# Performance work log

Measured on AMD Instinct MI355X. Metric: run time of the kernel, lower is better.

## Reference

```python
import jax, jax.numpy as jnp
import numpy as np

NUM_NODES = 25
EMBED_DIM = 64
OUT_SIZE = 2
N_TOTAL = 204800   # 8192 graphs * 25 nodes
N_EDGES = 3276800  # avg degree 16


def setup_inputs() -> dict:
    key = jax.random.key(0)
    ks = jax.random.split(key, 8)
    x = jax.random.normal(ks[0], (N_TOTAL, EMBED_DIM), dtype=jnp.float32)
    # random edges; real graphs are graph-local but math is identical
    edge_index = jax.random.randint(ks[1], (2, N_EDGES), 0, N_TOTAL, dtype=jnp.int32)
    batch = jnp.repeat(jnp.arange(N_TOTAL // NUM_NODES, dtype=jnp.int32), NUM_NODES)
    hid = NUM_NODES * EMBED_DIM  # 1600
    W_conv = jax.random.normal(ks[2], (EMBED_DIM, EMBED_DIM), dtype=jnp.float32) / np.sqrt(EMBED_DIM)
    b_conv = jnp.zeros((EMBED_DIM,), dtype=jnp.float32)
    W1 = jax.random.normal(ks[3], (hid, hid), dtype=jnp.float32) / np.sqrt(hid)
    b1 = jnp.zeros((hid,), dtype=jnp.float32)
    W2 = jax.random.normal(ks[4], (hid, OUT_SIZE), dtype=jnp.float32) / np.sqrt(hid)
    b2 = jnp.zeros((OUT_SIZE,), dtype=jnp.float32)
    return {"x": x, "edge_index": edge_index, "batch": batch,
            "W_conv": W_conv, "b_conv": b_conv,
            "W1": W1, "b1": b1, "W2": W2, "b2": b2}


def reference(x, edge_index, batch, W_conv, b_conv, W1, b1, W2, b2):
    N = x.shape[0]
    # --- GCNConv: add self-loops, symmetric degree norm, transform, scatter-add ---
    loop = jnp.arange(N, dtype=edge_index.dtype)
    src = jnp.concatenate([edge_index[0], loop])
    dst = jnp.concatenate([edge_index[1], loop])
    deg = jax.ops.segment_sum(jnp.ones_like(dst, dtype=x.dtype), dst, num_segments=N)
    dinv = jax.lax.rsqrt(deg)  # deg >= 1 due to self-loops
    norm = dinv[src] * dinv[dst]                       # [E+N]
    h = x @ W_conv                                     # [N, D]
    msg = h[src] * norm[:, None]                       # gather + scale
    h = jax.ops.segment_sum(msg, dst, num_segments=N) + b_conv
    h = jax.nn.relu(h)
    # --- dense head ---
    nb = -(-batch.shape[0] // NUM_NODES)               # ceil
    h = h.reshape(nb, NUM_NODES * EMBED_DIM)           # [B, 1600]
    h = jax.nn.relu(h @ W1 + b1)
    logits = h @ W2 + b2
    return jax.nn.softmax(logits, axis=-1)
```

## Files before the change

### kernel.cpp

```cpp
#include <hip/hip_runtime.h>
#include <hip/hip_bf16.h>
#include <stdint.h>

#define NT   204800
#define NE   3276800
#define ED   64
#define NBG  8192
#define HID  1600
#define CAP  44
#define NBKT 400
#define BCAP 9216
#define EPB  (NE / 512)

typedef float  f32x4  __attribute__((ext_vector_type(4)));
typedef __bf16 bf16x8 __attribute__((ext_vector_type(8)));
typedef int    i32x4  __attribute__((ext_vector_type(4)));

__device__ __forceinline__ void async_ld16(const void* g, void* l) {
    __builtin_amdgcn_global_load_lds(
        (__attribute__((address_space(1))) const void*)g,
        (__attribute__((address_space(3))) void*)l, 16, 0, 0);
}

__device__ __forceinline__ unsigned short f2bf_raw(float f) {
    __hip_bfloat16 h = __float2bfloat16(f);
    return *(unsigned short*)&h;
}

__global__ void k_initg(int* __restrict__ gcur, const float* __restrict__ Wc,
                        unsigned short* __restrict__ WcT) {
    int t = threadIdx.x;
    if (t < NBKT) gcur[t] = t * BCAP;
    for (int i = t; i < ED * ED; i += 512) {
        int k = i >> 6, n = i & 63;
        WcT[n * 64 + (((k >> 3) ^ (n & 7)) << 3) + (k & 7)] = f2bf_raw(Wc[i]);
    }
}

__global__ __launch_bounds__(256) void k_part(const int* __restrict__ srcv,
                                              const int* __restrict__ dstv,
                                              int* __restrict__ gcur,
                                              unsigned* __restrict__ rec) {
    __shared__ int hist[NBKT];
    __shared__ int scanA[NBKT];
    __shared__ int scanB[NBKT];
    __shared__ int gofs[NBKT];
    __shared__ unsigned buf[EPB];
    __shared__ unsigned short bkt[EPB];
    const int t = threadIdx.x;
    const int base = blockIdx.x * EPB;
    for (int i = t; i < NBKT; i += 256) hist[i] = 0;
    __syncthreads();
    unsigned keep[25];
#pragma unroll
    for (int j = 0; j < 25; ++j) {
        int d = dstv[base + j * 256 + t];
        int b = d >> 9;
        int ls = atomicAdd(&hist[b], 1);
        keep[j] = ((unsigned)ls << 18) | ((unsigned)(d & 511) << 9) | (unsigned)b;
    }
    __syncthreads();
    for (int i = t; i < NBKT; i += 256) gofs[i] = atomicAdd(&gcur[i], hist[i]);
    for (int i = t; i < NBKT; i += 256) scanA[i] = hist[i];
    __syncthreads();
    int* sp = scanA; int* dp = scanB;
    for (int off = 1; off < NBKT; off <<= 1) {
        for (int i = t; i < NBKT; i += 256)
            dp[i] = sp[i] + ((i >= off) ? sp[i - off] : 0);
        __syncthreads();
        int* tmp = sp; sp = dp; dp = tmp;
    }
    for (int i = t; i < NBKT; i += 256) dp[i] = sp[i] - hist[i];
    __syncthreads();
#pragma unroll
    for (int j = 0; j < 25; ++j) {
        int s = srcv[base + j * 256 + t];
        unsigned k = keep[j];
        int b   = (int)(k & 511u);
        int rel = (int)((k >> 9) & 511u);
        int ls  = (int)(k >> 18);
        int li  = dp[b] + ls;
        buf[li] = ((unsigned)s << 9) | (unsigned)rel;
        bkt[li] = (unsigned short)b;
    }
    __syncthreads();
    for (int i = t; i < EPB; i += 256) {
        int b = bkt[i];
        int idx = gofs[b] + (i - dp[b]);
        if (idx < (b + 1) * BCAP)
            rec[idx] = buf[i];
    }
}

__global__ __launch_bounds__(256) void k_fillb(const int* __restrict__ gcur,
                                               const unsigned* __restrict__ rec,
                                               int* __restrict__ cur,
                                               int* __restrict__ csr,
                                               float* __restrict__ dinv) {
    __shared__ int cnt[256];
    __shared__ int loc[256 * CAP];
    const int t = threadIdx.x;
    const int b = blockIdx.x >> 1;
    const int h = blockIdx.x & 1;
    const int n0 = b * 512 + h * 256;
    cnt[t] = 0;
    __syncthreads();
    const int bstart = b * BCAP;
    int bcnt = gcur[b] - bstart;
    bcnt = (bcnt > BCAP) ? BCAP : bcnt;
    for (int idx = t; idx < bcnt; idx += 256) {
        unsigned r = rec[bstart + idx];
        int rel = (int)(r & 511u);
        if ((rel >> 8) == h) {
            int rl = rel & 255;
            int ls = atomicAdd(&cnt[rl], 1);
            if (ls < CAP) loc[rl * CAP + ls] = (int)(r >> 9);
        }
    }
    __syncthreads();
    i32x4* gout = (i32x4*)(csr + (size_t)n0 * CAP);
    const i32x4* lin = (const i32x4*)loc;
    for (int i = t; i < 256 * CAP / 4; i += 256) gout[i] = lin[i];
    int cn = cnt[t];
    cur[n0 + t] = cn;
    dinv[n0 + t] = rsqrtf((float)cn + 1.f);
}

__global__ __launch_bounds__(256) void k_gemm_conv(const float* __restrict__ x,
                                                   const unsigned short* __restrict__ WcT,
                                                   const float* __restrict__ dinv,
                                                   __hip_bfloat16* __restrict__ hbs) {
    __shared__ unsigned short Xs[64 * 72];
    __shared__ unsigned short Wt[64 * 64];
    const int t = threadIdx.x;
    const int row0 = blockIdx.x * 64;
    async_ld16(WcT + (size_t)t * 8, &Wt[t * 8]);
    async_ld16(WcT + 2048 + (size_t)t * 8, &Wt[2048 + t * 8]);
#pragma unroll
    for (int i = 0; i < 4; ++i) {
        int idx = i * 256 + t;
        int r = idx >> 4, c4 = (idx & 15) << 2;
        f32x4 xv = ((const f32x4*)(x + (size_t)row0 * 64))[idx];
        ushort4 p;
        p.x = f2bf_raw(xv.x);
        p.y = f2bf_raw(xv.y);
        p.z = f2bf_raw(xv.z);
        p.w = f2bf_raw(xv.w);
        *(ushort4*)&Xs[r * 72 + c4] = p;
    }
    __syncthreads();
    const int w = t >> 6, lane = t & 63;
    const int fr = lane & 15, fq = lane >> 4;
    const int sw = fr & 7;
    f32x4 acc[4] = {};
#pragma unroll
    for (int kb = 0; kb < 2; ++kb) {
        bf16x8 av = *(const bf16x8*)&Xs[(w * 16 + fr) * 72 + kb * 32 + fq * 8];
#pragma unroll
        for (int j = 0; j < 4; ++j) {
            bf16x8 bv = *(const bf16x8*)&Wt[(j * 16 + fr) * 64 + (((kb << 2) + fq) ^ sw) * 8];
            acc[j] = __builtin_amdgcn_mfma_f32_16x16x32_bf16(av, bv, acc[j], 0, 0, 0);
        }
    }
#pragma unroll
    for (int r = 0; r < 4; ++r) {
        int row = row0 + w * 16 + fq * 4 + r;
        float di = dinv[row];
        unsigned short* dst = (unsigned short*)&hbs[(size_t)row * 64];
#pragma unroll
        for (int j = 0; j < 4; ++j)
            dst[j * 16 + fr] = f2bf_raw(acc[j][r] * di);
    }
}

__global__ __launch_bounds__(256) void k_gather(const int* __restrict__ cur,
                                                const int* __restrict__ csr,
                                                const float* __restrict__ dinv,
                                                const __hip_bfloat16* __restrict__ hbs,
                                                const float* __restrict__ bc,
                                                __hip_bfloat16* __restrict__ Hb) {
    const int lane = threadIdx.x & 63;
    const int du = __builtin_amdgcn_readfirstlane(blockIdx.x * 4 + (threadIdx.x >> 6));
    const float di = dinv[du];
    int cn = cur[du];
    cn = (cn > CAP) ? CAP : cn;
    const int* __restrict__ lst = csr + (size_t)du * CAP;
    const float self = __bfloat162float(hbs[(size_t)du * ED + lane]);
    float acc = self;
    int e = 0;
    for (; e + 16 <= cn; e += 16) {
#pragma unroll
        for (int q = 0; q < 16; ++q) {
            int s = lst[e + q];
            acc += __bfloat162float(hbs[(size_t)s * ED + lane]);
        }
    }
    if (e < cn) {
        const int pad = e + 16 - cn;
#pragma unroll
        for (int q = 0; q < 16; ++q) {
            int s = (e + q < cn) ? lst[e + q] : du;
            acc += __bfloat162float(hbs[(size_t)s * ED + lane]);
        }
        acc = fmaf(-(float)pad, self, acc);
    }
    Hb[(size_t)du * ED + lane] = __float2bfloat16(fmaxf(bc[lane] + di * acc, 0.f));
}

__global__ void k_convW1(const float* __restrict__ W1, __hip_bfloat16* __restrict__ Bt,
                         float* __restrict__ logits) {
    __shared__ float tile[64][65];
    const int t = threadIdx.x;
    const int k0 = blockIdx.x * 64;
    const int n0 = blockIdx.y * 64;
    if (blockIdx.x == 0 && blockIdx.y == 0)
        for (int i = t; i < 2 * NBG; i += 256) logits[i] = 0.f;
#pragma unroll
    for (int i = 0; i < 16; ++i) {
        int lin = i * 256 + t;
        int r = lin >> 6, c = lin & 63;
        tile[r][c] = W1[(size_t)(k0 + r) * HID + n0 + c];
    }
    __syncthreads();
#pragma unroll
    for (int i = 0; i < 16; ++i) {
        int lin = i * 256 + t;
        int nn = lin >> 6, kk = lin & 63;
        Bt[(size_t)(n0 + nn) * HID + k0 + kk] = __float2bfloat16(tile[kk][nn]);
    }
}

__global__ __launch_bounds__(128) void k_gemm1(const __hip_bfloat16* __restrict__ A,
                                               const __hip_bfloat16* __restrict__ Bt,
                                               const float* __restrict__ b1,
                                               const float* __restrict__ W2,
                                               float* __restrict__ logits) {
    __shared__ unsigned short As[2][128 * 64];
    __shared__ unsigned short Bs[2][64 * 64];
    const int t = threadIdx.x;
    const int lane = t & 63;
    const int w = t >> 6;
    const int lin = blockIdx.x;
    const int xc  = lin & 7;
    const int pos = lin >> 3;
    const int bm0 = (xc * 8 + (pos & 7)) * 128;
    const int bn0 = (pos >> 3) * 64;
    const int fr = lane & 15;
    const int fq = lane >> 4;
    const int lrow  = lane >> 3;
    const int lslot = (lane & 7) ^ lrow;
    const size_t soff = (size_t)lrow * HID + lslot * 8;
    const __hip_bfloat16* pa = A  + (size_t)bm0 * HID + soff;
    const __hip_bfloat16* pb = Bt + (size_t)bn0 * HID + soff;
    const int ra  = (w * 64 + fr) * 64;
    const int rb  = fr * 64;
    const int sl0 = ((0 + fq) ^ (fr & 7)) * 8;
    const int sl1 = ((4 + fq) ^ (fr & 7)) * 8;
    f32x4 acc[4][4] = {};

    auto STAGE = [&](int bidx) {
        unsigned short* dA = &As[bidx][(w * 8) * 512 + lane * 8];
        const __hip_bfloat16* sA = pa + (size_t)(w * 8) * 8 * HID;
#pragma unroll
        for (int q = 0; q < 8; ++q)
            async_ld16(sA + (size_t)q * 8 * HID, dA + q * 512);
        unsigned short* dB = &Bs[bidx][(w * 4) * 512 + lane * 8];
        const __hip_bfloat16* sB = pb + (size_t)(w * 4) * 8 * HID;
#pragma unroll
        for (int q = 0; q < 4; ++q)
            async_ld16(sB + (size_t)q * 8 * HID, dB + q * 512);
        pa += 64; pb += 64;
    };

    const int NKT = HID / 64;
    STAGE(0);
    STAGE(1);
    for (int kt = 0; kt < NKT; ++kt) {
        const int p = kt & 1;
        if (kt < NKT - 1)
            asm volatile("s_waitcnt vmcnt(12)\n\ts_barrier" ::: "memory");
        else
            asm volatile("s_waitcnt vmcnt(0)\n\ts_barrier" ::: "memory");
        bf16x8 av0[4], av1[4], bv0[4], bv1[4];
#pragma unroll
        for (int i = 0; i < 4; ++i) {
            av0[i] = *(const bf16x8*)&As[p][ra + i * 16 * 64 + sl0];
            av1[i] = *(const bf16x8*)&As[p][ra + i * 16 * 64 + sl1];
        }
#pragma unroll
        for (int j = 0; j < 4; ++j) {
            bv0[j] = *(const bf16x8*)&Bs[p][rb + j * 16 * 64 + sl0];
            bv1[j] = *(const bf16x8*)&Bs[p][rb + j * 16 * 64 + sl1];
        }
        __builtin_amdgcn_s_setprio(1);
#pragma unroll
        for (int i = 0; i < 4; ++i)
#pragma unroll
            for (int j = 0; j < 4; ++j) {
                acc[i][j] = __builtin_amdgcn_mfma_f32_16x16x32_bf16(av0[i], bv0[j], acc[i][j], 0, 0, 0);
                acc[i][j] = __builtin_amdgcn_mfma_f32_16x16x32_bf16(av1[i], bv1[j], acc[i][j], 0, 0, 0);
            }
        __builtin_amdgcn_s_setprio(0);
        if (kt < NKT - 2) {
            asm volatile("s_waitcnt lgkmcnt(0)\n\ts_barrier" ::: "memory");
            STAGE(p);
        }
    }

    float2 w2l[4];
    float  bl[4];
#pragma unroll
    for (int j = 0; j < 4; ++j) {
        int n = bn0 + j * 16 + fr;
        w2l[j] = ((const float2*)W2)[n];
        bl[j]  = b1[n];
    }
#pragma unroll
    for (int i = 0; i < 4; ++i) {
#pragma unroll
        for (int r = 0; r < 4; ++r) {
            float p0 = 0.f, p1 = 0.f;
#pragma unroll
            for (int j = 0; j < 4; ++j) {
                float hh = fmaxf(acc[i][j][r] + bl[j], 0.f);
                p0 = fmaf(hh, w2l[j].x, p0);
                p1 = fmaf(hh, w2l[j].y, p1);
            }
#pragma unroll
            for (int m = 1; m < 16; m <<= 1) {
                p0 += __shfl_xor(p0, m, 16);
                p1 += __shfl_xor(p1, m, 16);
            }
            if (fr == 0) {
                int mm = bm0 + w * 64 + i * 16 + fq * 4 + r;
                atomicAdd(&logits[mm * 2],     p0);
                atomicAdd(&logits[mm * 2 + 1], p1);
            }
        }
    }
}

__global__ void k_smax(const float* __restrict__ logits, const float* __restrict__ b2,
                       float* __restrict__ out) {
    int g = blockIdx.x * 256 + threadIdx.x;
    float l0 = logits[2 * g] + b2[0], l1 = logits[2 * g + 1] + b2[1];
    float mx = fmaxf(l0, l1);
    float e0 = expf(l0 - mx), e1 = expf(l1 - mx);
    float s = e0 + e1;
    out[2 * g]     = e0 / s;
    out[2 * g + 1] = e1 / s;
}

extern "C" void kernel_launch(void* const* d_in, const int* in_sizes, int n_in,
                              void* d_out, int out_size, void* d_ws, size_t ws_size,
                              hipStream_t stream) {
    const float* x  = (const float*)d_in[0];
    const int*   ei = (const int*)d_in[1];
    const float* Wc = (const float*)d_in[3];
    const float* bc = (const float*)d_in[4];
    const float* W1 = (const float*)d_in[5];
    const float* b1 = (const float*)d_in[6];
    const float* W2 = (const float*)d_in[7];
    const float* b2 = (const float*)d_in[8];
    float* out = (float*)d_out;

    const int* srcv = ei;
    const int* dstv = ei + NE;

    char* ws = (char*)d_ws;
    int*   cur  = (int*)ws;
    float* dinv = (float*)(ws + 819200);
    int*   gcur = (int*)(ws + 1638400);
    int*   csr  = (int*)(ws + 1642496);
    unsigned* rec = (unsigned*)(ws + 47517696);
    float* logits = (float*)(ws + 47517696);
    __hip_bfloat16* hbs = (__hip_bfloat16*)(ws + 47517696);
    __hip_bfloat16* Hb  = (__hip_bfloat16*)(ws + 73732096);
    __hip_bfloat16* Bt  = (__hip_bfloat16*)(ws + 99946496);
    unsigned short* WcT = (unsigned short*)(ws + 105066496);

    k_initg    <<<1, 512, 0, stream>>>(gcur, Wc, WcT);
    k_part     <<<512, 256, 0, stream>>>(srcv, dstv, gcur, rec);
    k_fillb    <<<NBKT * 2, 256, 0, stream>>>(gcur, rec, cur, csr, dinv);
    k_gemm_conv<<<NT / 64, 256, 0, stream>>>(x, WcT, dinv, hbs);
    k_gather   <<<NT / 4, 256, 0, stream>>>(cur, csr, dinv, hbs, bc, Hb);
    k_convW1   <<<dim3(HID / 64, HID / 64), 256, 0, stream>>>(W1, Bt, logits);
    k_gemm1    <<<1600, 128, 0, stream>>>(Hb, Bt, b1, W2, logits);
    k_smax     <<<NBG / 256, 256, 0, stream>>>(logits, b2, out);
}
```

Before: 357.7 us.

## Merge partition with conv GEMM and gather with W1 conversion into shared launches

Partition and the conv GEMM now run as one launch, split by block index. The source-side dinv scaling moves out of the GEMM and into the gather, so the GEMM no longer waits on degree computation and can overlap with edge partitioning. The gather and the W1 transpose/convert are likewise merged into one launch, which cuts the kernel count and lets independent work fill idle CUs. The partition scatter is rewritten to write per-bucket runs wave by wave, and the setprio hints in gemm1 are dropped. Running partition and conv together needs a separate workspace region for rec, with a fallback path when the workspace is too small. The gather now does an extra dinv load per edge.

```diff
diff --git a/kernel.cpp b/kernel.cpp
--- a/kernel.cpp
+++ b/kernel.cpp
@@ -37,18 +37,17 @@
     }
 }
 
-__global__ __launch_bounds__(256) void k_part(const int* __restrict__ srcv,
-                                              const int* __restrict__ dstv,
-                                              int* __restrict__ gcur,
-                                              unsigned* __restrict__ rec) {
-    __shared__ int hist[NBKT];
-    __shared__ int scanA[NBKT];
-    __shared__ int scanB[NBKT];
-    __shared__ int gofs[NBKT];
-    __shared__ unsigned buf[EPB];
-    __shared__ unsigned short bkt[EPB];
-    const int t = threadIdx.x;
-    const int base = blockIdx.x * EPB;
+__device__ __forceinline__ void dev_part(char* smem, int bid, int t,
+                                         const int* __restrict__ srcv,
+                                         const int* __restrict__ dstv,
+                                         int* __restrict__ gcur,
+                                         unsigned* __restrict__ rec) {
+    int* hist  = (int*)smem;
+    int* scanA = (int*)(smem + 1600);
+    int* scanB = (int*)(smem + 3200);
+    int* gofs  = (int*)(smem + 4800);
+    unsigned* buf = (unsigned*)(smem + 6400);
+    const int base = bid * EPB;
     for (int i = t; i < NBKT; i += 256) hist[i] = 0;
     __syncthreads();
     unsigned keep[25];
@@ -77,19 +76,90 @@
         int s = srcv[base + j * 256 + t];
         unsigned k = keep[j];
         int b   = (int)(k & 511u);
-        int rel = (int)((k >> 9) & 511u);
         int ls  = (int)(k >> 18);
-        int li  = dp[b] + ls;
-        buf[li] = ((unsigned)s << 9) | (unsigned)rel;
-        bkt[li] = (unsigned short)b;
-    }
-    __syncthreads();
-    for (int i = t; i < EPB; i += 256) {
-        int b = bkt[i];
-        int idx = gofs[b] + (i - dp[b]);
-        if (idx < (b + 1) * BCAP)
-            rec[idx] = buf[i];
-    }
+        buf[dp[b] + ls] = ((unsigned)s << 9) | (k >> 9 & 511u);
+    }
+    __syncthreads();
+    const int wv = t >> 6, ln = t & 63;
+    for (int b = wv; b < NBKT; b += 4) {
+        int st = dp[b], len = hist[b], go = gofs[b], cap = (b + 1) * BCAP;
+        for (int l = ln; l < len; l += 64) {
+            int idx = go + l;
+            if (idx < cap) rec[idx] = buf[st + l];
+        }
+    }
+}
+
+__device__ __forceinline__ void dev_conv(char* smem, int cb, int t,
+                                         const float* __restrict__ x,
+                                         const unsigned short* __restrict__ WcT,
+                                         __hip_bfloat16* __restrict__ hbs) {
+    unsigned short* Xs = (unsigned short*)smem;
+    unsigned short* Wt = (unsigned short*)(smem + 9216);
+    const int row0 = cb * 64;
+    async_ld16(WcT + (size_t)t * 8, &Wt[t * 8]);
+    async_ld16(WcT + 2048 + (size_t)t * 8, &Wt[2048 + t * 8]);
+#pragma unroll
+    for (int i = 0; i < 4; ++i) {
+        int idx = i * 256 + t;
+        int r = idx >> 4, c4 = (idx & 15) << 2;
+        f32x4 xv = ((const f32x4*)(x + (size_t)row0 * 64))[idx];
+        ushort4 p;
+        p.x = f2bf_raw(xv.x);
+        p.y = f2bf_raw(xv.y);
+        p.z = f2bf_raw(xv.z);
+        p.w = f2bf_raw(xv.w);
+        *(ushort4*)&Xs[r * 72 + c4] = p;
+    }
+    __syncthreads();
+    const int w = t >> 6, lane = t & 63;
+    const int fr = lane & 15, fq = lane >> 4;
+    const int sw = fr & 7;
+    f32x4 acc[4] = {};
+#pragma unroll
+    for (int kb = 0; kb < 2; ++kb) {
+        bf16x8 av = *(const bf16x8*)&Xs[(w * 16 + fr) * 72 + kb * 32 + fq * 8];
+#pragma unroll
+        for (int j = 0; j < 4; ++j) {
+            bf16x8 bv = *(const bf16x8*)&Wt[(j * 16 + fr) * 64 + (((kb << 2) + fq) ^ sw) * 8];
+            acc[j] = __builtin_amdgcn_mfma_f32_16x16x32_bf16(av, bv, acc[j], 0, 0, 0);
+        }
+    }
+#pragma unroll
+    for (int r = 0; r < 4; ++r) {
+        int row = row0 + w * 16 + fq * 4 + r;
+        unsigned short* dst = (unsigned short*)&hbs[(size_t)row * 64];
+#pragma unroll
+        for (int j = 0; j < 4; ++j)
+            dst[j * 16 + fr] = f2bf_raw(acc[j][r]);
+    }
+}
+
+__global__ __launch_bounds__(256) void k_pcv(const int* __restrict__ srcv,
+                                             const int* __restrict__ dstv,
+                                             int* __restrict__ gcur,
+                                             unsigned* __restrict__ rec,
+                                             const float* __restrict__ x,
+                                             const unsigned short* __restrict__ WcT,
+                                             __hip_bfloat16* __restrict__ hbs) {
+    __shared__ __attribute__((aligned(16))) char smem[32000];
+    const int t = threadIdx.x;
+    if (blockIdx.x < 512) dev_part(smem, blockIdx.x, t, srcv, dstv, gcur, rec);
+    else                  dev_conv(smem, blockIdx.x - 512, t, x, WcT, hbs);
+}
+
+__global__ __launch_bounds__(256) void k_part_s(const int* __restrict__ srcv,
+                                                const int* __restrict__ dstv,
+                                                int* __restrict__ gcur,
+                                                unsigned* __restrict__ rec) {
+    __shared__ __attribute__((aligned(16))) char smem[32000];
+    dev_part(smem, blockIdx.x, threadIdx.x, srcv, dstv, gcur, rec);
+}
+__global__ __launch_bounds__(256) void k_conv_s(const float* __restrict__ x,
+                                                const unsigned short* __restrict__ WcT,
+                                                __hip_bfloat16* __restrict__ hbs) {
+    __shared__ __attribute__((aligned(16))) char smem[17408];
+    dev_conv(smem, blockIdx.x, threadIdx.x, x, WcT, hbs);
 }
 
 __global__ __launch_bounds__(256) void k_fillb(const int* __restrict__ gcur,
@@ -126,73 +196,27 @@
     dinv[n0 + t] = rsqrtf((float)cn + 1.f);
 }
 
-__global__ __launch_bounds__(256) void k_gemm_conv(const float* __restrict__ x,
-                                                   const unsigned short* __restrict__ WcT,
-                                                   const float* __restrict__ dinv,
-                                                   __hip_bfloat16* __restrict__ hbs) {
-    __shared__ unsigned short Xs[64 * 72];
-    __shared__ unsigned short Wt[64 * 64];
-    const int t = threadIdx.x;
-    const int row0 = blockIdx.x * 64;
-    async_ld16(WcT + (size_t)t * 8, &Wt[t * 8]);
-    async_ld16(WcT + 2048 + (size_t)t * 8, &Wt[2048 + t * 8]);
-#pragma unroll
-    for (int i = 0; i < 4; ++i) {
-        int idx = i * 256 + t;
-        int r = idx >> 4, c4 = (idx & 15) << 2;
-        f32x4 xv = ((const f32x4*)(x + (size_t)row0 * 64))[idx];
-        ushort4 p;
-        p.x = f2bf_raw(xv.x);
-        p.y = f2bf_raw(xv.y);
-        p.z = f2bf_raw(xv.z);
-        p.w = f2bf_raw(xv.w);
-        *(ushort4*)&Xs[r * 72 + c4] = p;
-    }
-    __syncthreads();
-    const int w = t >> 6, lane = t & 63;
-    const int fr = lane & 15, fq = lane >> 4;
-    const int sw = fr & 7;
-    f32x4 acc[4] = {};
-#pragma unroll
-    for (int kb = 0; kb < 2; ++kb) {
-        bf16x8 av = *(const bf16x8*)&Xs[(w * 16 + fr) * 72 + kb * 32 + fq * 8];
-#pragma unroll
-        for (int j = 0; j < 4; ++j) {
-            bf16x8 bv = *(const bf16x8*)&Wt[(j * 16 + fr) * 64 + (((kb << 2) + fq) ^ sw) * 8];
-            acc[j] = __builtin_amdgcn_mfma_f32_16x16x32_bf16(av, bv, acc[j], 0, 0, 0);
-        }
-    }
-#pragma unroll
-    for (int r = 0; r < 4; ++r) {
-        int row = row0 + w * 16 + fq * 4 + r;
-        float di = dinv[row];
-        unsigned short* dst = (unsigned short*)&hbs[(size_t)row * 64];
-#pragma unroll
-        for (int j = 0; j < 4; ++j)
-            dst[j * 16 + fr] = f2bf_raw(acc[j][r] * di);
-    }
-}
-
-__global__ __launch_bounds__(256) void k_gather(const int* __restrict__ cur,
-                                                const int* __restrict__ csr,
-                                                const float* __restrict__ dinv,
-                                                const __hip_bfloat16* __restrict__ hbs,
-                                                const float* __restrict__ bc,
-                                                __hip_bfloat16* __restrict__ Hb) {
-    const int lane = threadIdx.x & 63;
-    const int du = __builtin_amdgcn_readfirstlane(blockIdx.x * 4 + (threadIdx.x >> 6));
+__device__ __forceinline__ void dev_gather(int bid, int t,
+                                           const int* __restrict__ cur,
+                                           const int* __restrict__ csr,
+                                           const float* __restrict__ dinv,
+                                           const __hip_bfloat16* __restrict__ hbs,
+                                           const float* __restrict__ bc,
+                                           __hip_bfloat16* __restrict__ Hb) {
+    const int lane = t & 63;
+    const int du = __builtin_amdgcn_readfirstlane(bid * 4 + (t >> 6));
     const float di = dinv[du];
     int cn = cur[du];
     cn = (cn > CAP) ? CAP : cn;
     const int* __restrict__ lst = csr + (size_t)du * CAP;
-    const float self = __bfloat162float(hbs[(size_t)du * ED + lane]);
-    float acc = self;
+    const float selfs = __bfloat162float(hbs[(size_t)du * ED + lane]) * di;
+    float acc = selfs;
     int e = 0;
     for (; e + 16 <= cn; e += 16) {
 #pragma unroll
         for (int q = 0; q < 16; ++q) {
             int s = lst[e + q];
-            acc += __bfloat162float(hbs[(size_t)s * ED + lane]);
+            acc = fmaf(__bfloat162float(hbs[(size_t)s * ED + lane]), dinv[s], acc);
         }
     }
     if (e < cn) {
@@ -200,20 +224,21 @@
 #pragma unroll
         for (int q = 0; q < 16; ++q) {
             int s = (e + q < cn) ? lst[e + q] : du;
-            acc += __bfloat162float(hbs[(size_t)s * ED + lane]);
-        }
-        acc = fmaf(-(float)pad, self, acc);
+            acc = fmaf(__bfloat162float(hbs[(size_t)s * ED + lane]), dinv[s], acc);
+        }
+        acc = fmaf(-(float)pad, selfs, acc);
     }
     Hb[(size_t)du * ED + lane] = __float2bfloat16(fmaxf(bc[lane] + di * acc, 0.f));
 }
 
-__global__ void k_convW1(const float* __restrict__ W1, __hip_bfloat16* __restrict__ Bt,
-                         float* __restrict__ logits) {
+__device__ __forceinline__ void dev_convW1(int cb, int t,
+                                           const float* __restrict__ W1,
+                                           __hip_bfloat16* __restrict__ Bt,
+                                           float* __restrict__ logits) {
     __shared__ float tile[64][65];
-    const int t = threadIdx.x;
-    const int k0 = blockIdx.x * 64;
-    const int n0 = blockIdx.y * 64;
-    if (blockIdx.x == 0 && blockIdx.y == 0)
+    const int k0 = (cb % 25) * 64;
+    const int n0 = (cb / 25) * 64;
+    if (cb == 0)
         for (int i = t; i < 2 * NBG; i += 256) logits[i] = 0.f;
 #pragma unroll
     for (int i = 0; i < 16; ++i) {
@@ -228,6 +253,20 @@
         int nn = lin >> 6, kk = lin & 63;
         Bt[(size_t)(n0 + nn) * HID + k0 + kk] = __float2bfloat16(tile[kk][nn]);
     }
+}
+
+__global__ __launch_bounds__(256) void k_gcw(const int* __restrict__ cur,
+                                             const int* __restrict__ csr,
+                                             const float* __restrict__ dinv,
+                                             const __hip_bfloat16* __restrict__ hbs,
+                                             const float* __restrict__ bc,
+                                             __hip_bfloat16* __restrict__ Hb,
+                                             const float* __restrict__ W1,
+                                             __hip_bfloat16* __restrict__ Bt,
+                                             float* __restrict__ logits) {
+    const int t = threadIdx.x;
+    if (blockIdx.x < NT / 4) dev_gather(blockIdx.x, t, cur, csr, dinv, hbs, bc, Hb);
+    else                     dev_convW1(blockIdx.x - NT / 4, t, W1, Bt, logits);
 }
 
 __global__ __launch_bounds__(128) void k_gemm1(const __hip_bfloat16* __restrict__ A,
@@ -292,7 +331,6 @@
             bv0[j] = *(const bf16x8*)&Bs[p][rb + j * 16 * 64 + sl0];
             bv1[j] = *(const bf16x8*)&Bs[p][rb + j * 16 * 64 + sl1];
         }
-        __builtin_amdgcn_s_setprio(1);
 #pragma unroll
         for (int i = 0; i < 4; ++i)
 #pragma unroll
@@ -300,7 +338,6 @@
                 acc[i][j] = __builtin_amdgcn_mfma_f32_16x16x32_bf16(av0[i], bv0[j], acc[i][j], 0, 0, 0);
                 acc[i][j] = __builtin_amdgcn_mfma_f32_16x16x32_bf16(av1[i], bv1[j], acc[i][j], 0, 0, 0);
             }
-        __builtin_amdgcn_s_setprio(0);
         if (kt < NKT - 2) {
             asm volatile("s_waitcnt lgkmcnt(0)\n\ts_barrier" ::: "memory");
             STAGE(p);
@@ -372,19 +409,29 @@
     float* dinv = (float*)(ws + 819200);
     int*   gcur = (int*)(ws + 1638400);
     int*   csr  = (int*)(ws + 1642496);
-    unsigned* rec = (unsigned*)(ws + 47517696);
-    float* logits = (float*)(ws + 47517696);
     __hip_bfloat16* hbs = (__hip_bfloat16*)(ws + 47517696);
     __hip_bfloat16* Hb  = (__hip_bfloat16*)(ws + 73732096);
     __hip_bfloat16* Bt  = (__hip_bfloat16*)(ws + 99946496);
     unsigned short* WcT = (unsigned short*)(ws + 105066496);
-
-    k_initg    <<<1, 512, 0, stream>>>(gcur, Wc, WcT);
-    k_part     <<<512, 256, 0, stream>>>(srcv, dstv, gcur, rec);
-    k_fillb    <<<NBKT * 2, 256, 0, stream>>>(gcur, rec, cur, csr, dinv);
-    k_gemm_conv<<<NT / 64, 256, 0, stream>>>(x, WcT, dinv, hbs);
-    k_gather   <<<NT / 4, 256, 0, stream>>>(cur, csr, dinv, hbs, bc, Hb);
-    k_convW1   <<<dim3(HID / 64, HID / 64), 256, 0, stream>>>(W1, Bt, logits);
-    k_gemm1    <<<1600, 128, 0, stream>>>(Hb, Bt, b1, W2, logits);
-    k_smax     <<<NBG / 256, 256, 0, stream>>>(logits, b2, out);
-}
+    float* logits = (float*)(ws + 105074688);
+
+    const size_t REC_HI_END = 105140224ull + (size_t)NBKT * BCAP * 4;
+    if (ws_size >= REC_HI_END) {
+        unsigned* rec = (unsigned*)(ws + 105140224);
+        k_initg<<<1, 512, 0, stream>>>(gcur, Wc, WcT);
+        k_pcv  <<<512 + NT / 64, 256, 0, stream>>>(srcv, dstv, gcur, rec, x, WcT, hbs);
+        k_fillb<<<NBKT * 2, 256, 0, stream>>>(gcur, rec, cur, csr, dinv);
+        k_gcw  <<<NT / 4 + 625, 256, 0, stream>>>(cur, csr, dinv, hbs, bc, Hb, W1, Bt, logits);
+        k_gemm1<<<1600, 128, 0, stream>>>(Hb, Bt, b1, W2, logits);
+        k_smax <<<NBG / 256, 256, 0, stream>>>(logits, b2, out);
+    } else {
+        unsigned* rec = (unsigned*)(ws + 47517696);
+        k_initg <<<1, 512, 0, stream>>>(gcur, Wc, WcT);
+        k_part_s<<<512, 256, 0, stream>>>(srcv, dstv, gcur, rec);
+        k_fillb <<<NBKT * 2, 256, 0, stream>>>(gcur, rec, cur, csr, dinv);
+        k_conv_s<<<NT / 64, 256, 0, stream>>>(x, WcT, hbs);
+        k_gcw   <<<NT / 4 + 625, 256, 0, stream>>>(cur, csr, dinv, hbs, bc, Hb, W1, Bt, logits);
+        k_gemm1 <<<1600, 128, 0, stream>>>(Hb, Bt, b1, W2, logits);
+        k_smax  <<<NBG / 256, 256, 0, stream>>>(logits, b2, out);
+    }
+}
```

Measured after the change: 405.1 us. +13.3%, slower.
